# Kernel optimization log

Hardware: AMD Instinct MI355X
Metric: run time of the kernel (lower is better)

## Reference

```python
import jax, jax.numpy as jnp
import numpy as np

N, D = 262144, 128      # samples, features
K = 512                 # n_clusters
ITERS = 10              # max_iter


def setup_inputs() -> dict:
    key = jax.random.key(0)
    X = jax.random.normal(key, (N, D), dtype=jnp.float32)
    return {"X": X}


def _assign(X, C):
    # Squared Euclidean distances; argmin is invariant to the sqrt in the
    # original EuclideanDistance, so labels are identical.
    # d2[n, k] = ||x_n||^2 - 2 x_n . c_k + ||c_k||^2
    d2 = (jnp.sum(X * X, axis=1, keepdims=True)
          - 2.0 * (X @ C.T)
          + jnp.sum(C * C, axis=1))
    return jnp.argmin(d2, axis=1)  # [N] int32


def reference(X):
    C0 = X[:K, :]  # centroids initialized to first K samples (clone/detach)

    def step(C, _):
        labels = _assign(X, C)                                   # [N]
        sums = jax.ops.segment_sum(X, labels, num_segments=K)    # [K, D]
        counts = jax.ops.segment_sum(jnp.ones((N,), X.dtype), labels,
                                     num_segments=K)             # [K]
        # mean over empty cluster -> 0/0 = NaN, matching torch's mean of
        # an empty selection.
        Cn = sums / counts[:, None]
        return Cn, labels

    _, labels_all = jax.lax.scan(step, C0, None, length=ITERS)
    return labels_all[-1]  # labels from the final iteration, [N]
```

## Files before the change

### kernel.cpp

```cpp
#include <hip/hip_runtime.h>

#define NP 262144
#define DI 128
#define KCL 512
#define NIT 10
#define NCH 1024
#define CHS 256

__device__ __forceinline__ bool isnan_bits32(float x) {
  unsigned b = __float_as_uint(x);
  return (b & 0x7FFFFFFFu) > 0x7F800000u;
}

__device__ __forceinline__ float np_pairwise128_sq(const float* v) {
  float r[8];
  #pragma unroll
  for (int j = 0; j < 8; ++j) r[j] = __fmul_rn(v[j], v[j]);
  #pragma unroll
  for (int t = 1; t < 16; ++t)
    #pragma unroll
    for (int j = 0; j < 8; ++j)
      r[j] = __fadd_rn(r[j], __fmul_rn(v[8 * t + j], v[8 * t + j]));
  float t01 = __fadd_rn(r[0], r[1]), t23 = __fadd_rn(r[2], r[3]);
  float t45 = __fadd_rn(r[4], r[5]), t67 = __fadd_rn(r[6], r[7]);
  return __fadd_rn(__fadd_rn(t01, t23), __fadd_rn(t45, t67));
}

__global__ void k_init(const float* __restrict__ X, float* __restrict__ C,
                       float* __restrict__ cnorm) {
  int k = blockIdx.x, d = threadIdx.x;
  float v = X[(size_t)k * DI + d];
  C[(size_t)k * DI + d] = v;
  __shared__ float row[DI];
  row[d] = v;
  __syncthreads();
  if (d == 0) cnorm[k] = np_pairwise128_sq(row);
}

__global__ void k_xnorm(const float* __restrict__ X, float* __restrict__ xnorm) {
  const int p = blockIdx.x * 256 + threadIdx.x;
  const float4* X4 = (const float4*)X + (size_t)p * 32;
  float r[8];
  {
    float4 q0 = X4[0], q1 = X4[1];
    r[0] = __fmul_rn(q0.x, q0.x); r[1] = __fmul_rn(q0.y, q0.y);
    r[2] = __fmul_rn(q0.z, q0.z); r[3] = __fmul_rn(q0.w, q0.w);
    r[4] = __fmul_rn(q1.x, q1.x); r[5] = __fmul_rn(q1.y, q1.y);
    r[6] = __fmul_rn(q1.z, q1.z); r[7] = __fmul_rn(q1.w, q1.w);
  }
  #pragma unroll
  for (int t = 1; t < 16; ++t) {
    float4 q0 = X4[2 * t], q1 = X4[2 * t + 1];
    r[0] = __fadd_rn(r[0], __fmul_rn(q0.x, q0.x));
    r[1] = __fadd_rn(r[1], __fmul_rn(q0.y, q0.y));
    r[2] = __fadd_rn(r[2], __fmul_rn(q0.z, q0.z));
    r[3] = __fadd_rn(r[3], __fmul_rn(q0.w, q0.w));
    r[4] = __fadd_rn(r[4], __fmul_rn(q1.x, q1.x));
    r[5] = __fadd_rn(r[5], __fmul_rn(q1.y, q1.y));
    r[6] = __fadd_rn(r[6], __fmul_rn(q1.z, q1.z));
    r[7] = __fadd_rn(r[7], __fmul_rn(q1.w, q1.w));
  }
  float t01 = __fadd_rn(r[0], r[1]), t23 = __fadd_rn(r[2], r[3]);
  float t45 = __fadd_rn(r[4], r[5]), t67 = __fadd_rn(r[6], r[7]);
  xnorm[p] = __fadd_rn(__fadd_rn(t01, t23), __fadd_rn(t45, t67));
}

__global__ __launch_bounds__(256, 2)
void k_assign_q(const float* __restrict__ X, const float* __restrict__ C,
                const float* __restrict__ cnorm, const float* __restrict__ xnorm,
                int* __restrict__ labels) {
  __shared__ __align__(16) float Xs[128][36];
  __shared__ __align__(16) float Cs[128][36];
  const int tid = threadIdx.x;
  const int tx = tid & 15, ty = tid >> 4;
  const int row0 = blockIdx.x * 128;
  const float4* X4 = (const float4*)X;
  const float4* C4 = (const float4*)C;

  float xn[8];
  #pragma unroll
  for (int r = 0; r < 8; ++r) xn[r] = xnorm[row0 + ty + 16 * r];

  float best[8];
  int bestk[8], fnan[8];
  #pragma unroll
  for (int r = 0; r < 8; ++r) { best[r] = 0.0f; bestk[r] = -1; fnan[r] = 0x7fffffff; }

  for (int kc = 0; kc < 4; ++kc) {
    float acc[8][8];
    #pragma unroll
    for (int r = 0; r < 8; ++r)
      #pragma unroll
      for (int j = 0; j < 8; ++j) acc[r][j] = 0.0f;

    for (int dc = 0; dc < 4; ++dc) {
      __syncthreads();
      #pragma unroll
      for (int i = 0; i < 4; ++i) {
        int idx = tid + 256 * i, p = idx >> 3, q = idx & 7;
        *(float4*)&Xs[p][q * 4] = X4[(size_t)(row0 + p) * 32 + dc * 8 + q];
        *(float4*)&Cs[p][q * 4] = C4[(size_t)(kc * 128 + p) * 32 + dc * 8 + q];
      }
      __syncthreads();
      for (int dq = 0; dq < 8; ++dq) {
        float4 xv[8], cv[8];
        #pragma unroll
        for (int r = 0; r < 8; ++r) xv[r] = *(const float4*)&Xs[ty + 16 * r][dq * 4];
        #pragma unroll
        for (int j = 0; j < 8; ++j) cv[j] = *(const float4*)&Cs[j * 16 + tx][dq * 4];
        #pragma unroll
        for (int r = 0; r < 8; ++r)
          #pragma unroll
          for (int j = 0; j < 8; ++j) {
            acc[r][j] = __fmaf_rn(xv[r].x, cv[j].x, acc[r][j]);
            acc[r][j] = __fmaf_rn(xv[r].y, cv[j].y, acc[r][j]);
            acc[r][j] = __fmaf_rn(xv[r].z, cv[j].z, acc[r][j]);
            acc[r][j] = __fmaf_rn(xv[r].w, cv[j].w, acc[r][j]);
          }
      }
    }
    #pragma unroll
    for (int r = 0; r < 8; ++r) {
      #pragma unroll
      for (int j = 0; j < 8; ++j) {
        int k = kc * 128 + j * 16 + tx;
        float s = __fadd_rn(__fsub_rn(xn[r], __fmul_rn(2.0f, acc[r][j])), cnorm[k]);
        if (isnan_bits32(s)) {
          if (k < fnan[r]) fnan[r] = k;
        } else if (bestk[r] < 0 || s < best[r]) {
          best[r] = s; bestk[r] = k;
        }
      }
    }
  }
  #pragma unroll
  for (int r = 0; r < 8; ++r) {
    float b = best[r]; int bk = bestk[r]; int fn = fnan[r];
    #pragma unroll
    for (int m = 8; m; m >>= 1) {
      float ob = __shfl_xor(b, m, 64);
      int obk = __shfl_xor(bk, m, 64);
      int ofn = __shfl_xor(fn, m, 64);
      if (ofn < fn) fn = ofn;
      bool take = (obk >= 0) && (bk < 0 || ob < b || (ob == b && obk < bk));
      if (take) { b = ob; bk = obk; }
    }
    if (tx == 0) labels[row0 + ty + 16 * r] = (fn != 0x7fffffff) ? fn : bk;
  }
}


__global__ void k_hist(const int* __restrict__ labels, int* __restrict__ counts) {
  __shared__ int hist[KCL];
  int c = blockIdx.x, t = threadIdx.x;
  hist[t] = 0; hist[t + 256] = 0;
  __syncthreads();
  int lab = labels[c * CHS + t];
  atomicAdd(&hist[lab], 1);
  __syncthreads();
  counts[(size_t)t * NCH + c] = hist[t];
  counts[(size_t)(t + 256) * NCH + c] = hist[t + 256];
}

__global__ void k_scan_chunks(const int* __restrict__ counts, int* __restrict__ cbase,
                              int* __restrict__ total) {
  __shared__ int s[NCH];
  int k = blockIdx.x, c = threadIdx.x;
  int v = counts[(size_t)k * NCH + c];
  s[c] = v;
  __syncthreads();
  for (int off = 1; off < NCH; off <<= 1) {
    int t = (c >= off) ? s[c - off] : 0;
    __syncthreads();
    s[c] += t;
    __syncthreads();
  }
  cbase[(size_t)k * NCH + c] = s[c] - v;
  if (c == NCH - 1) total[k] = s[c];
}

__global__ void k_scan_k(const int* __restrict__ total, int* __restrict__ offset) {
  __shared__ int s[KCL];
  int c = threadIdx.x;
  int v = total[c];
  s[c] = v;
  __syncthreads();
  for (int off = 1; off < KCL; off <<= 1) {
    int t = (c >= off) ? s[c - off] : 0;
    __syncthreads();
    s[c] += t;
    __syncthreads();
  }
  offset[c] = s[c] - v;
}

__global__ void k_scatter(const int* __restrict__ labels, const int* __restrict__ cbase,
                          const int* __restrict__ offset, int* __restrict__ list) {
  __shared__ int lab[CHS];
  int c = blockIdx.x, t = threadIdx.x;
  int L = labels[c * CHS + t];
  lab[t] = L;
  __syncthreads();
  int rank = 0;
  for (int j = 0; j < t; ++j) rank += (lab[j] == L);
  list[offset[L] + cbase[(size_t)L * NCH + c] + rank] = c * CHS + t;
}

__global__ void k_sum(const float* __restrict__ X, const int* __restrict__ list,
                      const int* __restrict__ offset, const int* __restrict__ total,
                      float* __restrict__ C, float* __restrict__ cnorm) {
  int k = blockIdx.x, d = threadIdx.x;
  int n = total[k], off = offset[k];
  float acc = 0.0f;
  int t = 0;
  for (; t + 4 <= n; t += 4) {
    int i0 = list[off + t + 0], i1 = list[off + t + 1];
    int i2 = list[off + t + 2], i3 = list[off + t + 3];
    float x0 = X[(size_t)i0 * DI + d], x1 = X[(size_t)i1 * DI + d];
    float x2 = X[(size_t)i2 * DI + d], x3 = X[(size_t)i3 * DI + d];
    acc = __fadd_rn(acc, x0); acc = __fadd_rn(acc, x1);
    acc = __fadd_rn(acc, x2); acc = __fadd_rn(acc, x3);
  }
  for (; t < n; ++t) {
    int i = list[off + t];
    acc = __fadd_rn(acc, X[(size_t)i * DI + d]);
  }
  float cv = (n == 0) ? __uint_as_float(0x7FC00000u) : __fdiv_rn(acc, (float)n);
  C[(size_t)k * DI + d] = cv;
  __shared__ float row[DI];
  row[d] = cv;
  __syncthreads();
  if (d == 0) cnorm[k] = np_pairwise128_sq(row);
}

extern "C" void kernel_launch(void* const* d_in, const int* in_sizes, int n_in,
                              void* d_out, int out_size, void* d_ws, size_t ws_size,
                              hipStream_t stream) {
  (void)in_sizes; (void)n_in; (void)out_size; (void)ws_size;
  const float* X = (const float*)d_in[0];
  int* out = (int*)d_out;
  char* ws = (char*)d_ws;
  float* C      = (float*)(ws);
  float* cnorm  = (float*)(ws + 262144);
  float* xnorm  = (float*)(ws + 264192);
  int*   counts = (int*)(ws + 264192 + 1048576);
  int*   cbase  = (int*)(ws + 264192 + 1048576 + 2097152);
  int*   total  = (int*)(ws + 264192 + 1048576 + 2 * 2097152);
  int*   offset = (int*)(ws + 264192 + 1048576 + 2 * 2097152 + 2048);
  int*   list   = (int*)(ws + 264192 + 1048576 + 2 * 2097152 + 4096);

  k_init<<<KCL, DI, 0, stream>>>(X, C, cnorm);
  k_xnorm<<<NP / 256, 256, 0, stream>>>(X, xnorm);
  for (int t = 0; t < NIT; ++t) {
    k_assign_q<<<NP / 128, 256, 0, stream>>>(X, C, cnorm, xnorm, out);
    if (t < NIT - 1) {
      k_hist<<<NCH, CHS, 0, stream>>>(out, counts);
      k_scan_chunks<<<KCL, NCH, 0, stream>>>(counts, cbase, total);
      k_scan_k<<<1, KCL, 0, stream>>>(total, offset);
      k_scatter<<<NCH, CHS, 0, stream>>>(out, cbase, offset, list);
      k_sum<<<KCL, DI, 0, stream>>>(X, list, offset, total, C, cnorm);
    }
  }
}
```

Before: 6.105 ms.

## Double-buffer assign kernel tiles with direct global-to-LDS loads and XOR swizzle

The distance/argmin kernel now keeps two LDS buffers and prefetches the next X/C tile with global_load_lds (direct global-to-LDS DMA) while computing on the current one. The padded layout is replaced by an XOR-swizzled layout to avoid bank conflicts, and the inner loop streams centroid vectors one at a time to cut register pressure. This removes one barrier per phase and hides load latency, at the cost of more LDS and reliance on the builtin's per-wave placement semantics for correctness.

Measured after the change: 9.150 ms. +49.9%, slower.

```diff
diff --git a/kernel.cpp b/kernel.cpp
--- a/kernel.cpp
+++ b/kernel.cpp
@@ -6,6 +6,9 @@
 #define NIT 10
 #define NCH 1024
 #define CHS 256
+
+#define GLBC(p) ((const __attribute__((address_space(1))) void*)(p))
+#define LDSC(p) ((__attribute__((address_space(3))) void*)(p))
 
 __device__ __forceinline__ bool isnan_bits32(float x) {
   unsigned b = __float_as_uint(x);
@@ -66,17 +69,33 @@
 }
 
 __global__ __launch_bounds__(256, 2)
-void k_assign_q(const float* __restrict__ X, const float* __restrict__ C,
+void k_assign_a(const float* __restrict__ X, const float* __restrict__ C,
                 const float* __restrict__ cnorm, const float* __restrict__ xnorm,
                 int* __restrict__ labels) {
-  __shared__ __align__(16) float Xs[128][36];
-  __shared__ __align__(16) float Cs[128][36];
+  __shared__ __align__(16) float Xs[2][128][32];
+  __shared__ __align__(16) float Cs[2][128][32];
   const int tid = threadIdx.x;
   const int tx = tid & 15, ty = tid >> 4;
   const int row0 = blockIdx.x * 128;
+  const int wave = tid >> 6;
+  const int lane = tid & 63;
+  const int srow = lane >> 3;
+  const int squad = lane & 7;
   const float4* X4 = (const float4*)X;
   const float4* C4 = (const float4*)C;
 
+  #define STAGE(b, KC, DC) { \
+    _Pragma("unroll") \
+    for (int m = 0; m < 4; ++m) { \
+      int rbase = m * 32 + wave * 8; \
+      __builtin_amdgcn_global_load_lds( \
+        GLBC(&X4[(size_t)(row0 + rbase + srow) * 32 + (DC) * 8 + (squad ^ srow)]), \
+        LDSC(&Xs[b][rbase][0]), 16, 0, 0); \
+      __builtin_amdgcn_global_load_lds( \
+        GLBC(&C4[(size_t)((KC) * 128 + rbase + srow) * 32 + (DC) * 8 + (squad ^ srow)]), \
+        LDSC(&Cs[b][rbase][0]), 16, 0, 0); \
+    } }
+
   float xn[8];
   #pragma unroll
   for (int r = 0; r < 8; ++r) xn[r] = xnorm[row0 + ty + 16 * r];
@@ -85,6 +104,12 @@
   int bestk[8], fnan[8];
   #pragma unroll
   for (int r = 0; r < 8; ++r) { best[r] = 0.0f; bestk[r] = -1; fnan[r] = 0x7fffffff; }
+
+  STAGE(0, 0, 0);
+  __syncthreads();
+  int cur = 0;
+  const int txs = (tx & 7);
+  const int tys = (ty & 7);
 
   for (int kc = 0; kc < 4; ++kc) {
     float acc[8][8];
@@ -94,30 +119,31 @@
       for (int j = 0; j < 8; ++j) acc[r][j] = 0.0f;
 
     for (int dc = 0; dc < 4; ++dc) {
-      __syncthreads();
+      int ph = kc * 4 + dc;
+      if (ph < 15) {
+        int np1 = ph + 1;
+        STAGE(cur ^ 1, np1 >> 2, np1 & 3);
+      }
       #pragma unroll
-      for (int i = 0; i < 4; ++i) {
-        int idx = tid + 256 * i, p = idx >> 3, q = idx & 7;
-        *(float4*)&Xs[p][q * 4] = X4[(size_t)(row0 + p) * 32 + dc * 8 + q];
-        *(float4*)&Cs[p][q * 4] = C4[(size_t)(kc * 128 + p) * 32 + dc * 8 + q];
+      for (int dq = 0; dq < 8; ++dq) {
+        float4 xv[8];
+        #pragma unroll
+        for (int r = 0; r < 8; ++r)
+          xv[r] = *(const float4*)&Xs[cur][ty + 16 * r][(dq ^ tys) * 4];
+        #pragma unroll
+        for (int j = 0; j < 8; ++j) {
+          float4 cv = *(const float4*)&Cs[cur][j * 16 + tx][(dq ^ txs) * 4];
+          #pragma unroll
+          for (int r = 0; r < 8; ++r) {
+            acc[r][j] = __fmaf_rn(xv[r].x, cv.x, acc[r][j]);
+            acc[r][j] = __fmaf_rn(xv[r].y, cv.y, acc[r][j]);
+            acc[r][j] = __fmaf_rn(xv[r].z, cv.z, acc[r][j]);
+            acc[r][j] = __fmaf_rn(xv[r].w, cv.w, acc[r][j]);
+          }
+        }
       }
       __syncthreads();
-      for (int dq = 0; dq < 8; ++dq) {
-        float4 xv[8], cv[8];
-        #pragma unroll
-        for (int r = 0; r < 8; ++r) xv[r] = *(const float4*)&Xs[ty + 16 * r][dq * 4];
-        #pragma unroll
-        for (int j = 0; j < 8; ++j) cv[j] = *(const float4*)&Cs[j * 16 + tx][dq * 4];
-        #pragma unroll
-        for (int r = 0; r < 8; ++r)
-          #pragma unroll
-          for (int j = 0; j < 8; ++j) {
-            acc[r][j] = __fmaf_rn(xv[r].x, cv[j].x, acc[r][j]);
-            acc[r][j] = __fmaf_rn(xv[r].y, cv[j].y, acc[r][j]);
-            acc[r][j] = __fmaf_rn(xv[r].z, cv[j].z, acc[r][j]);
-            acc[r][j] = __fmaf_rn(xv[r].w, cv[j].w, acc[r][j]);
-          }
-      }
+      cur ^= 1;
     }
     #pragma unroll
     for (int r = 0; r < 8; ++r) {
@@ -133,6 +159,7 @@
       }
     }
   }
+  #undef STAGE
   #pragma unroll
   for (int r = 0; r < 8; ++r) {
     float b = best[r]; int bk = bestk[r]; int fn = fnan[r];
@@ -252,7 +279,7 @@
   k_init<<<KCL, DI, 0, stream>>>(X, C, cnorm);
   k_xnorm<<<NP / 256, 256, 0, stream>>>(X, xnorm);
   for (int t = 0; t < NIT; ++t) {
-    k_assign_q<<<NP / 128, 256, 0, stream>>>(X, C, cnorm, xnorm, out);
+    k_assign_a<<<NP / 128, 256, 0, stream>>>(X, C, cnorm, xnorm, out);
     if (t < NIT - 1) {
       k_hist<<<NCH, CHS, 0, stream>>>(out, counts);
       k_scan_chunks<<<KCL, NCH, 0, stream>>>(counts, cbase, total);
```
